# Kernel tuning notes

Measured on AMD Instinct MI355X. Metric: run time of the kernel, lower is better.

Reference implementation:

```python
import jax, jax.numpy as jnp
import numpy as np

N_NODES = 40000
N_EDGES = 320000
IN_DIM = 256
HID = 128
HEADS = 4
N_GAT = 3  # num_layers - 1
EPS = 1e-5
NEG_SLOPE = 0.2  # PyG GATConv default


def setup_inputs() -> dict:
    key = jax.random.key(0)
    ks = jax.random.split(key, 16)
    s = 0.05
    return {
        "x": jax.random.normal(ks[0], (N_NODES, IN_DIM), jnp.float32),
        "edge_index": jax.random.randint(ks[1], (2, N_EDGES), 0, N_NODES, jnp.int64),
        "proj_W": jax.random.normal(ks[2], (IN_DIM, HID), jnp.float32) * s,
        "proj_b": jnp.zeros((HID,), jnp.float32),
        "gat_W": jax.random.normal(ks[3], (N_GAT, HID, HEADS * HID), jnp.float32) * s,
        "gat_att_src": jax.random.normal(ks[4], (N_GAT, HEADS, HID), jnp.float32) * s,
        "gat_att_dst": jax.random.normal(ks[5], (N_GAT, HEADS, HID), jnp.float32) * s,
        "gat_bias": jnp.zeros((N_GAT, HID), jnp.float32),
        "ln_gamma": jnp.ones((N_GAT, HID), jnp.float32),
        "ln_beta": jnp.zeros((N_GAT, HID), jnp.float32),
        "gcn_W": jax.random.normal(ks[6], (HID, 1), jnp.float32) * s,
        "gcn_b": jnp.zeros((1,), jnp.float32),
    }


def reference(x, edge_index, proj_W, proj_b, gat_W, gat_att_src, gat_att_dst,
              gat_bias, ln_gamma, ln_beta, gcn_W, gcn_b):
    N = x.shape[0]
    loops = jnp.arange(N)
    src = jnp.concatenate([edge_index[0], loops])  # add_self_loops=True
    dst = jnp.concatenate([edge_index[1], loops])

    h = x @ proj_W + proj_b  # [N, HID]

    for i in range(N_GAT):
        identity = h
        xh = (h @ gat_W[i]).reshape(N, HEADS, HID)      # [N, H, C]
        a_s = jnp.einsum("nhc,hc->nh", xh, gat_att_src[i])  # [N, H]
        a_d = jnp.einsum("nhc,hc->nh", xh, gat_att_dst[i])
        e = jax.nn.leaky_relu(a_s[src] + a_d[dst], NEG_SLOPE)  # [E, H]
        # segment softmax over incoming edges per dst node
        m = jax.ops.segment_max(e, dst, num_segments=N)
        ex = jnp.exp(e - m[dst])
        denom = jax.ops.segment_sum(ex, dst, num_segments=N)
        alpha = ex / denom[dst]                         # [E, H]
        agg = jax.ops.segment_sum(xh[src] * alpha[:, :, None], dst, num_segments=N)
        h = agg.mean(axis=1) + gat_bias[i]              # concat=False -> head mean
        # LayerNorm (biased variance, eps=1e-5)
        mu = h.mean(-1, keepdims=True)
        var = ((h - mu) ** 2).mean(-1, keepdims=True)
        h = (h - mu) * jax.lax.rsqrt(var + EPS) * ln_gamma[i] + ln_beta[i]
        h = jax.nn.relu(h)
        # dropout: inference mode -> identity
        h = h + identity

    # GCNConv(hidden, 1) with symmetric normalization and self loops
    deg = jax.ops.segment_sum(jnp.ones_like(dst, dtype=h.dtype), dst, num_segments=N)
    dinv = jax.lax.rsqrt(deg)  # deg >= 1 due to self loops
    norm = dinv[src] * dinv[dst]                        # [E]
    xw = h @ gcn_W                                      # [N, 1]
    out = jax.ops.segment_sum(xw[src] * norm[:, None], dst, num_segments=N) + gcn_b
    return jax.nn.sigmoid(out).reshape(-1)
```

## Files before the change

kernel.cpp:

```cpp
#include <hip/hip_runtime.h>
#include <math.h>

#define INDIM 256
#define HID 128
#define HEADS 4
#define NGAT 3
#define LN_EPS 1e-5f
#define SLOPE 0.2f
#define MPAD 40064
#define LOG2E 1.4426950408889634f

typedef __attribute__((ext_vector_type(8))) short short8;
typedef __attribute__((ext_vector_type(4))) float f32x4;

__device__ inline float wsum(float v) {
#pragma unroll
  for (int m = 1; m < 64; m <<= 1) v += __shfl_xor(v, m, 64);
  return v;
}
__device__ inline float wmax(float v) {
#pragma unroll
  for (int m = 1; m < 64; m <<= 1) v = fmaxf(v, __shfl_xor(v, m, 64));
  return v;
}
__device__ inline float lk2(float v) { return fmaxf(v, SLOPE * v) * LOG2E; }
__device__ inline float sel4(float a0, float a1, float a2, float a3, int i) {
  float lo = (i & 1) ? a1 : a0;
  float hi = (i & 1) ? a3 : a2;
  return (i & 2) ? hi : lo;
}

__device__ inline unsigned short f2b(float f) {
  unsigned u = __float_as_uint(f);
  unsigned r = (u + 0x7FFFu + ((u >> 16) & 1u)) >> 16;
  return (unsigned short)r;
}
__device__ inline void unp8(const uint4 v, float f[8]) {
  f[0] = __uint_as_float(v.x << 16);
  f[1] = __uint_as_float(v.x & 0xFFFF0000u);
  f[2] = __uint_as_float(v.y << 16);
  f[3] = __uint_as_float(v.y & 0xFFFF0000u);
  f[4] = __uint_as_float(v.z << 16);
  f[5] = __uint_as_float(v.z & 0xFFFF0000u);
  f[6] = __uint_as_float(v.w << 16);
  f[7] = __uint_as_float(v.w & 0xFFFF0000u);
}

__device__ __host__ inline size_t fidx(int row, int k, int K) {
  return ((size_t)(row >> 4) * (K >> 5) + (k >> 5)) * 512 +
         ((((k >> 3) & 3) * 16 + (row & 15)) << 3) + (k & 7);
}

__global__ void k_deg(const int* __restrict__ ei, int E, int N, int* __restrict__ deg) {
  int e = blockIdx.x * blockDim.x + threadIdx.x;
  if (e >= E + N) return;
  int dst = (e < E) ? ei[E + e] : (e - E);
  atomicAdd(&deg[dst], 1);
}

__global__ void k_scan1(const int* __restrict__ deg, int N, int* __restrict__ bsums) {
  __shared__ int s[256];
  int gid = blockIdx.x * 256 + threadIdx.x;
  s[threadIdx.x] = (gid < N) ? deg[gid] : 0;
  __syncthreads();
  for (int off = 128; off > 0; off >>= 1) {
    if (threadIdx.x < off) s[threadIdx.x] += s[threadIdx.x + off];
    __syncthreads();
  }
  if (threadIdx.x == 0) bsums[blockIdx.x] = s[0];
}

__global__ void k_scan2(int* __restrict__ bsums, int nblk, int* __restrict__ rowptr, int N) {
  __shared__ int s[256];
  int t = threadIdx.x;
  int v = (t < nblk) ? bsums[t] : 0;
  s[t] = v;
  __syncthreads();
  for (int off = 1; off < 256; off <<= 1) {
    int u = (t >= off) ? s[t - off] : 0;
    __syncthreads();
    s[t] += u;
    __syncthreads();
  }
  if (t < nblk) bsums[t] = s[t] - v;
  if (t == nblk - 1) rowptr[N] = s[t];
}

__global__ void k_scan3(const int* __restrict__ deg, int N, const int* __restrict__ bsums,
                        int* __restrict__ rowptr, int* __restrict__ cursor,
                        float* __restrict__ dinv) {
  __shared__ int s[256];
  int gid = blockIdx.x * 256 + threadIdx.x;
  int v = (gid < N) ? deg[gid] : 0;
  s[threadIdx.x] = v;
  __syncthreads();
  for (int off = 1; off < 256; off <<= 1) {
    int t = (threadIdx.x >= off) ? s[threadIdx.x - off] : 0;
    __syncthreads();
    s[threadIdx.x] += t;
    __syncthreads();
  }
  if (gid < N) {
    int ex = bsums[blockIdx.x] + s[threadIdx.x] - v;
    rowptr[gid] = ex;
    cursor[gid] = ex;
    dinv[gid] = rsqrtf((float)v);
  }
}

__global__ void k_fill(const int* __restrict__ ei, int E, int N,
                       int* __restrict__ cursor, int* __restrict__ csr) {
  int e = blockIdx.x * blockDim.x + threadIdx.x;
  if (e >= E + N) return;
  int src, dst;
  if (e < E) { src = ei[e]; dst = ei[E + e]; } else { src = dst = e - E; }
  int pos = atomicAdd(&cursor[dst], 1);
  csr[pos] = src;
}

__global__ void k_wtp(const float* __restrict__ W, unsigned short* __restrict__ Wt) {
  int idx = blockIdx.x * 256 + threadIdx.x;
  if (idx >= INDIM * HID) return;
  int k = idx >> 7, c = idx & 127;
  Wt[fidx(c, k, INDIM)] = f2b(W[idx]);
}

__global__ void k_wt2(const float* __restrict__ W, unsigned short* __restrict__ Wt) {
  int idx = blockIdx.x * 256 + threadIdx.x;
  if (idx >= NGAT * HID * HEADS * HID) return;
  int l = idx / (HID * HEADS * HID);
  int rem = idx - l * HID * HEADS * HID;
  int k = rem >> 9;
  int cc = rem & 511;
  int hh = cc >> 7, c = cc & 127;
  Wt[(size_t)l * (HID * HEADS * HID) + fidx(c, hh * HID + k, HEADS * HID)] =
      f2b(W[idx] * 0.25f);
}

__global__ void k_xfrag(const float* __restrict__ x, unsigned short* __restrict__ xbF,
                        int N) {
  int t = blockIdx.x * 256 + threadIdx.x;
  if (t >= MPAD * 32) return;
  int n = t >> 5, kc = t & 31;
  uint4 pk = make_uint4(0, 0, 0, 0);
  if (n < N) {
    const float* ap = x + (size_t)n * INDIM + kc * 8;
    float4 u = *(const float4*)ap;
    float4 v = *(const float4*)(ap + 4);
    pk.x = (unsigned)f2b(u.x) | ((unsigned)f2b(u.y) << 16);
    pk.y = (unsigned)f2b(u.z) | ((unsigned)f2b(u.w) << 16);
    pk.z = (unsigned)f2b(v.x) | ((unsigned)f2b(v.y) << 16);
    pk.w = (unsigned)f2b(v.z) | ((unsigned)f2b(v.w) << 16);
  }
  size_t addr = ((size_t)(n >> 4) * 8 + (kc >> 2)) * 512 +
                (((kc & 3) * 16 + (n & 15)) << 3);
  *(uint4*)(xbF + addr) = pk;
}

__global__ void k_wvec(const float* __restrict__ W, const float* __restrict__ atts,
                       const float* __restrict__ attd, float* __restrict__ w_s,
                       float* __restrict__ w_d) {
  int lane = threadIdx.x & 63;
  int idx = blockIdx.x * 4 + (threadIdx.x >> 6);
  if (idx >= NGAT * HEADS * HID) return;
  int l = idx / (HEADS * HID);
  int rem = idx - l * (HEADS * HID);
  int hh = rem >> 7, k = rem & 127;
  const float2 w2 = *(const float2*)(W + ((size_t)(l * HID + k)) * (HEADS * HID) +
                                     hh * HID + lane * 2);
  const float2 s2 = *(const float2*)(atts + (size_t)(l * HEADS + hh) * HID + lane * 2);
  const float2 d2 = *(const float2*)(attd + (size_t)(l * HEADS + hh) * HID + lane * 2);
  float ps = w2.x * s2.x + w2.y * s2.y;
  float pd = w2.x * d2.x + w2.y * d2.y;
  ps = wsum(ps);
  pd = wsum(pd);
  if (lane == 0) { w_s[idx] = ps; w_d[idx] = pd; }
}

__global__ __launch_bounds__(256) void k_mm(
    const unsigned short* __restrict__ xbF, const unsigned short* __restrict__ WtPF,
    const float* __restrict__ bias, const float* __restrict__ ws0,
    const float* __restrict__ wd0, float* __restrict__ h,
    unsigned short* __restrict__ hb, float* __restrict__ a_s,
    float* __restrict__ a_d) {
  const int wid = threadIdx.x >> 6;
  const int lane = threadIdx.x & 63;
  const int l15 = lane & 15;
  const int g = lane >> 4;
  const int row0 = blockIdx.x * 64 + wid * 16;
  f32x4 acc[8] = {};
  const unsigned short* Ap = xbF + (size_t)(row0 >> 4) * 8 * 512 + lane * 8;
  const unsigned short* Bp = WtPF + lane * 8;
  for (int kb = 0; kb < 8; ++kb) {
    short8 af = *(const short8*)(Ap + kb * 512);
    short8 bfr[8];
#pragma unroll
    for (int ni = 0; ni < 8; ++ni)
      bfr[ni] = *(const short8*)(Bp + (size_t)(ni * 8 + kb) * 512);
#pragma unroll
    for (int ni = 0; ni < 8; ++ni)
      acc[ni] = __builtin_amdgcn_mfma_f32_16x16x32_bf16(af, bfr[ni], acc[ni], 0, 0, 0);
  }
#pragma unroll
  for (int r = 0; r < 4; ++r) {
    const int row = row0 + g * 4 + r;
    float* hr = h + (size_t)row * HID;
    unsigned short* hbr = hb + (size_t)row * HID;
    float yv[8];
#pragma unroll
    for (int ni = 0; ni < 8; ++ni) {
      const int c = ni * 16 + l15;
      yv[ni] = acc[ni][r] + bias[c];
      hr[c] = yv[ni];
      hbr[c] = f2b(yv[ni]);
    }
    float ps[4], pd[4];
#pragma unroll
    for (int h4 = 0; h4 < 4; ++h4) {
      float pv = 0.f, qv = 0.f;
#pragma unroll
      for (int ni = 0; ni < 8; ++ni) {
        const int c = h4 * HID + ni * 16 + l15;
        pv = fmaf(yv[ni], ws0[c], pv);
        qv = fmaf(yv[ni], wd0[c], qv);
      }
#pragma unroll
      for (int m = 1; m < 16; m <<= 1) {
        pv += __shfl_xor(pv, m, 64);
        qv += __shfl_xor(qv, m, 64);
      }
      ps[h4] = pv;
      pd[h4] = qv;
    }
    if (l15 == 0) {
      *(float4*)(a_s + (size_t)row * 4) = make_float4(ps[0], ps[1], ps[2], ps[3]);
      *(float4*)(a_d + (size_t)row * 4) = make_float4(pd[0], pd[1], pd[2], pd[3]);
    }
  }
}

__global__ __launch_bounds__(256) void k_agg2(
    const int* __restrict__ rowptr, const int* __restrict__ csr,
    const unsigned short* __restrict__ hb, const float* __restrict__ a_s,
    const float* __restrict__ a_d, unsigned short* __restrict__ aggF, int N) {
  __shared__ int s_lds[4][64];
  __shared__ float al_lds[4][4][68];
  int lane = threadIdx.x & 63;
  int wid = threadIdx.x >> 6;
  int n = blockIdx.x * 4 + wid;
  if (n >= N) return;
  int beg = rowptr[n], end = rowptr[n + 1];
  int deg = end - beg;
  const float4 adv = *(const float4*)(a_d + (size_t)n * 4);
  const int g = lane >> 4;
  const int l15 = lane & 15;
  const unsigned short* hbase = hb + l15 * 8;
  float acc[8] = {};
  float f[8];
  if (deg <= 64) {
    int e = beg + lane;
    bool val = e < end;
    int s = csr[val ? e : end - 1];
    const float4 asv = *(const float4*)(a_s + (size_t)s * 4);
    float L0 = lk2(asv.x + adv.x);
    float L1 = lk2(asv.y + adv.y);
    float L2 = lk2(asv.z + adv.z);
    float L3 = lk2(asv.w + adv.w);
    float m0 = wmax(val ? L0 : -3e38f);
    float m1 = wmax(val ? L1 : -3e38f);
    float m2 = wmax(val ? L2 : -3e38f);
    float m3 = wmax(val ? L3 : -3e38f);
    float e0 = val ? exp2f(L0 - m0) : 0.f;
    float e1 = val ? exp2f(L1 - m1) : 0.f;
    float e2 = val ? exp2f(L2 - m2) : 0.f;
    float e3 = val ? exp2f(L3 - m3) : 0.f;
    s_lds[wid][lane] = s;
    al_lds[wid][0][lane] = e0 / wsum(e0);
    al_lds[wid][1][lane] = e1 / wsum(e1);
    al_lds[wid][2][lane] = e2 / wsum(e2);
    al_lds[wid][3][lane] = e3 / wsum(e3);
    asm volatile("s_waitcnt lgkmcnt(0)" ::: "memory");
    const int* sw = s_lds[wid];
    const float* aw = al_lds[wid][g];
    int nIter = (deg + 3) >> 2;
    for (int it = 0; it < nIter; ++it) {
      int4 s4 = *(const int4*)(sw + it * 4);
      float4 a4 = *(const float4*)(aw + it * 4);
      uint4 r0 = *(const uint4*)(hbase + (size_t)s4.x * HID);
      uint4 r1 = *(const uint4*)(hbase + (size_t)s4.y * HID);
      uint4 r2 = *(const uint4*)(hbase + (size_t)s4.z * HID);
      uint4 r3 = *(const uint4*)(hbase + (size_t)s4.w * HID);
      unp8(r0, f);
#pragma unroll
      for (int j = 0; j < 8; ++j) acc[j] = fmaf(a4.x, f[j], acc[j]);
      unp8(r1, f);
#pragma unroll
      for (int j = 0; j < 8; ++j) acc[j] = fmaf(a4.y, f[j], acc[j]);
      unp8(r2, f);
#pragma unroll
      for (int j = 0; j < 8; ++j) acc[j] = fmaf(a4.z, f[j], acc[j]);
      unp8(r3, f);
#pragma unroll
      for (int j = 0; j < 8; ++j) acc[j] = fmaf(a4.w, f[j], acc[j]);
    }
  } else {
    float m0 = -3e38f, m1 = -3e38f, m2 = -3e38f, m3 = -3e38f;
    for (int e = beg + lane; e < end; e += 64) {
      int s = csr[e];
      const float4 asv = *(const float4*)(a_s + (size_t)s * 4);
      m0 = fmaxf(m0, lk2(asv.x + adv.x));
      m1 = fmaxf(m1, lk2(asv.y + adv.y));
      m2 = fmaxf(m2, lk2(asv.z + adv.z));
      m3 = fmaxf(m3, lk2(asv.w + adv.w));
    }
    m0 = wmax(m0); m1 = wmax(m1); m2 = wmax(m2); m3 = wmax(m3);
    float d0 = 0.f, d1 = 0.f, d2 = 0.f, d3 = 0.f;
    for (int e = beg + lane; e < end; e += 64) {
      int s = csr[e];
      const float4 asv = *(const float4*)(a_s + (size_t)s * 4);
      d0 += exp2f(lk2(asv.x + adv.x) - m0);
      d1 += exp2f(lk2(asv.y + adv.y) - m1);
      d2 += exp2f(lk2(asv.z + adv.z) - m2);
      d3 += exp2f(lk2(asv.w + adv.w) - m3);
    }
    float r0 = 1.f / wsum(d0);
    float r1 = 1.f / wsum(d1);
    float r2 = 1.f / wsum(d2);
    float r3 = 1.f / wsum(d3);
    for (int sb = beg; sb < end; sb += 64) {
      int e = sb + lane;
      bool val = e < end;
      int s = csr[val ? e : end - 1];
      const float4 asv = *(const float4*)(a_s + (size_t)s * 4);
      float q0 = val ? exp2f(lk2(asv.x + adv.x) - m0) * r0 : 0.f;
      float q1 = val ? exp2f(lk2(asv.y + adv.y) - m1) * r1 : 0.f;
      float q2 = val ? exp2f(lk2(asv.z + adv.z) - m2) * r2 : 0.f;
      float q3 = val ? exp2f(lk2(asv.w + adv.w) - m3) * r3 : 0.f;
      int cnt = min(64, end - sb);
      for (int i = 0; i < cnt; ++i) {
        int si = __shfl(s, i, 64);
        float c0 = __shfl(q0, i, 64), c1 = __shfl(q1, i, 64);
        float c2 = __shfl(q2, i, 64), c3 = __shfl(q3, i, 64);
        uint4 hv = *(const uint4*)(hbase + (size_t)si * HID);
        float bi = sel4(c0, c1, c2, c3, g);
        unp8(hv, f);
#pragma unroll
        for (int j = 0; j < 8; ++j) acc[j] = fmaf(bi, f[j], acc[j]);
      }
    }
  }
  uint4 pk;
  pk.x = (unsigned)f2b(acc[0]) | ((unsigned)f2b(acc[1]) << 16);
  pk.y = (unsigned)f2b(acc[2]) | ((unsigned)f2b(acc[3]) << 16);
  pk.z = (unsigned)f2b(acc[4]) | ((unsigned)f2b(acc[5]) << 16);
  pk.w = (unsigned)f2b(acc[6]) | ((unsigned)f2b(acc[7]) << 16);
  size_t addr = ((size_t)(n >> 4) * 16 + (g * 4 + (l15 >> 2))) * 512 +
                (((l15 & 3) * 16 + (n & 15)) << 3);
  *(uint4*)(aggF + addr) = pk;
}

template <int ATT>
__global__ __launch_bounds__(256) void k_mm2(
    const unsigned short* __restrict__ aggF, const unsigned short* __restrict__ Bt,
    const float* __restrict__ bias, const float* __restrict__ gamma,
    const float* __restrict__ beta, const float* __restrict__ wsn,
    const float* __restrict__ wdn, float* __restrict__ h,
    unsigned short* __restrict__ hb, float* __restrict__ a_s,
    float* __restrict__ a_d, float* __restrict__ xw) {
  const int wid = threadIdx.x >> 6;
  const int lane = threadIdx.x & 63;
  const int l15 = lane & 15;
  const int g = lane >> 4;
  const int row0 = blockIdx.x * 64 + wid * 16;
  f32x4 acc[8] = {};
  const unsigned short* Ap = aggF + (size_t)(row0 >> 4) * 16 * 512 + lane * 8;
  const unsigned short* Bp = Bt + lane * 8;
  for (int kb = 0; kb < 16; ++kb) {
    short8 a0 = *(const short8*)(Ap + kb * 512);
    short8 bfr[8];
#pragma unroll
    for (int ni = 0; ni < 8; ++ni)
      bfr[ni] = *(const short8*)(Bp + (size_t)(ni * 16 + kb) * 512);
#pragma unroll
    for (int ni = 0; ni < 8; ++ni)
      acc[ni] = __builtin_amdgcn_mfma_f32_16x16x32_bf16(a0, bfr[ni], acc[ni], 0, 0, 0);
  }
  float gm[8], bt8[8];
#pragma unroll
  for (int ni = 0; ni < 8; ++ni) {
    int c = ni * 16 + l15;
    gm[ni] = gamma[c];
    bt8[ni] = beta[c];
    float bs = bias[c];
#pragma unroll
    for (int r = 0; r < 4; ++r) acc[ni][r] += bs;
  }
#pragma unroll
  for (int r = 0; r < 4; ++r) {
    float s = 0.f;
#pragma unroll
    for (int ni = 0; ni < 8; ++ni) s += acc[ni][r];
#pragma unroll
    for (int m = 1; m < 16; m <<= 1) s += __shfl_xor(s, m, 64);
    float mu = s * (1.f / 128.f);
    float q = 0.f;
#pragma unroll
    for (int ni = 0; ni < 8; ++ni) {
      float dd = acc[ni][r] - mu;
      q += dd * dd;
    }
#pragma unroll
    for (int m = 1; m < 16; m <<= 1) q += __shfl_xor(q, m, 64);
    float rstd = rsqrtf(q * (1.f / 128.f) + LN_EPS);
    const int row = row0 + g * 4 + r;
    float* hr = h + (size_t)row * HID;
    unsigned short* hbr = hb + (size_t)row * HID;
    float yv[8];
#pragma unroll
    for (int ni = 0; ni < 8; ++ni) {
      int c = ni * 16 + l15;
      float y = (acc[ni][r] - mu) * rstd * gm[ni] + bt8[ni];
      y = fmaxf(y, 0.f) + hr[c];
      hr[c] = y;
      hbr[c] = f2b(y);
      yv[ni] = y;
    }
    if (ATT == 1) {
      float ps[4], pd[4];
#pragma unroll
      for (int h4 = 0; h4 < 4; ++h4) {
        float pv = 0.f, qv = 0.f;
#pragma unroll
        for (int ni = 0; ni < 8; ++ni) {
          const int c = h4 * HID + ni * 16 + l15;
          pv = fmaf(yv[ni], wsn[c], pv);
          qv = fmaf(yv[ni], wdn[c], qv);
        }
#pragma unroll
        for (int m = 1; m < 16; m <<= 1) {
          pv += __shfl_xor(pv, m, 64);
          qv += __shfl_xor(qv, m, 64);
        }
        ps[h4] = pv;
        pd[h4] = qv;
      }
      if (l15 == 0) {
        *(float4*)(a_s + (size_t)row * 4) = make_float4(ps[0], ps[1], ps[2], ps[3]);
        *(float4*)(a_d + (size_t)row * 4) = make_float4(pd[0], pd[1], pd[2], pd[3]);
      }
    } else {
      float pv = 0.f;
#pragma unroll
      for (int ni = 0; ni < 8; ++ni) pv = fmaf(yv[ni], wsn[ni * 16 + l15], pv);
#pragma unroll
      for (int m = 1; m < 16; m <<= 1) pv += __shfl_xor(pv, m, 64);
      if (l15 == 0) xw[row] = pv;
    }
  }
}

__global__ __launch_bounds__(256) void k_gcn(const int* __restrict__ rowptr,
                                             const int* __restrict__ csr,
                                             const float* __restrict__ xw,
                                             const float* __restrict__ dinv,
                                             const float* __restrict__ gcn_b,
                                             float* __restrict__ out, int N) {
  int n = blockIdx.x * blockDim.x + threadIdx.x;
  if (n >= N) return;
  float acc = 0.f;
  int beg = rowptr[n], end = rowptr[n + 1];
  for (int e = beg; e < end; ++e) {
    int s = csr[e];
    acc += xw[s] * dinv[s];
  }
  float z = acc * dinv[n] + gcn_b[0];
  out[n] = 1.f / (1.f + expf(-z));
}

extern "C" void kernel_launch(void* const* d_in, const int* in_sizes, int n_in,
                              void* d_out, int out_size, void* d_ws, size_t ws_size,
                              hipStream_t stream) {
  const float* x = (const float*)d_in[0];
  const int* ei = (const int*)d_in[1];
  const float* proj_W = (const float*)d_in[2];
  const float* proj_b = (const float*)d_in[3];
  const float* gat_W = (const float*)d_in[4];
  const float* gat_as = (const float*)d_in[5];
  const float* gat_ad = (const float*)d_in[6];
  const float* gat_bias = (const float*)d_in[7];
  const float* ln_g = (const float*)d_in[8];
  const float* ln_b = (const float*)d_in[9];
  const float* gcn_W = (const float*)d_in[10];
  const float* gcn_b = (const float*)d_in[11];
  float* out = (float*)d_out;

  const int N = in_sizes[0] / INDIM;
  const int E = in_sizes[1] / 2;
  const int TOT = E + N;

  size_t off = 0;
  auto alloc = [&](size_t bytes) {
    void* p = (char*)d_ws + off;
    off += (bytes + 255) & ~(size_t)255;
    return p;
  };
  float* h = (float*)alloc((size_t)MPAD * HID * 4);
  unsigned short* hb = (unsigned short*)alloc((size_t)MPAD * HID * 2);
  unsigned short* aggF = (unsigned short*)alloc((size_t)MPAD * HEADS * HID * 2);
  unsigned short* xbF = (unsigned short*)alloc((size_t)MPAD * INDIM * 2);
  unsigned short* WtPF = (unsigned short*)alloc((size_t)HID * INDIM * 2);
  unsigned short* Wt2F = (unsigned short*)alloc((size_t)NGAT * HID * HEADS * HID * 2);
  float* w_s = (float*)alloc((size_t)NGAT * HEADS * HID * 4);
  float* w_d = (float*)alloc((size_t)NGAT * HEADS * HID * 4);
  float* a_s = (float*)alloc((size_t)MPAD * HEADS * 4);
  float* a_d = (float*)alloc((size_t)MPAD * HEADS * 4);
  int* deg = (int*)alloc((size_t)N * 4);
  int* rowptr = (int*)alloc((size_t)(N + 1) * 4);
  int* cursor = (int*)alloc((size_t)N * 4);
  int* csr = (int*)alloc((size_t)TOT * 4);
  int* bsums = (int*)alloc(1024);
  float* dinv = (float*)alloc((size_t)N * 4);
  float* xw = (float*)alloc((size_t)MPAD * 4);
  (void)ws_size;

  const int NBLK = (N + 255) / 256;
  const int EBLK = (TOT + 255) / 256;
  const int WBLK = (N + 3) / 4;

  hipMemsetAsync(deg, 0, (size_t)N * 4, stream);
  k_deg<<<EBLK, 256, 0, stream>>>(ei, E, N, deg);
  k_scan1<<<NBLK, 256, 0, stream>>>(deg, N, bsums);
  k_scan2<<<1, 256, 0, stream>>>(bsums, NBLK, rowptr, N);
  k_scan3<<<NBLK, 256, 0, stream>>>(deg, N, bsums, rowptr, cursor, dinv);
  k_fill<<<EBLK, 256, 0, stream>>>(ei, E, N, cursor, csr);

  k_wtp<<<(INDIM * HID + 255) / 256, 256, 0, stream>>>(proj_W, WtPF);
  k_wt2<<<(NGAT * HID * HEADS * HID + 255) / 256, 256, 0, stream>>>(gat_W, Wt2F);
  k_wvec<<<(NGAT * HEADS * HID + 3) / 4, 256, 0, stream>>>(gat_W, gat_as, gat_ad, w_s, w_d);
  k_xfrag<<<(MPAD * 32 + 255) / 256, 256, 0, stream>>>(x, xbF, N);

  hipMemsetAsync(aggF + (size_t)N * HEADS * HID, 0,
                 (size_t)(MPAD - N) * HEADS * HID * 2, stream);

  k_mm<<<MPAD / 64, 256, 0, stream>>>(xbF, WtPF, proj_b, w_s, w_d, h, hb, a_s, a_d);

  for (int i = 0; i < NGAT; ++i) {
    k_agg2<<<WBLK, 256, 0, stream>>>(rowptr, csr, hb, a_s, a_d, aggF, N);
    if (i < NGAT - 1) {
      k_mm2<1><<<MPAD / 64, 256, 0, stream>>>(
          aggF, Wt2F + (size_t)i * HID * HEADS * HID, gat_bias + (size_t)i * HID,
          ln_g + (size_t)i * HID, ln_b + (size_t)i * HID,
          w_s + (size_t)(i + 1) * HEADS * HID, w_d + (size_t)(i + 1) * HEADS * HID,
          h, hb, a_s, a_d, nullptr);
    } else {
      k_mm2<2><<<MPAD / 64, 256, 0, stream>>>(
          aggF, Wt2F + (size_t)i * HID * HEADS * HID, gat_bias + (size_t)i * HID,
          ln_g + (size_t)i * HID, ln_b + (size_t)i * HID, gcn_W, nullptr,
          h, hb, nullptr, nullptr, xw);
    }
  }

  k_gcn<<<NBLK, 256, 0, stream>>>(rowptr, csr, xw, dinv, gcn_b, out, N);
}
```

Baseline: 293.9 us.

## Split GAT aggregation into separate attention-softmax and feature-gather kernels

Replaces the fused per-node softmax+aggregation kernel with two kernels: one computes per-edge, per-head attention weights with one thread per (node, head) and writes them to a new global buffer, and a second gathers the bf16 source features weighted by those stored alphas. It also folds the two weight-preparation kernels into one launch and replaces the padding memset with zero writes from the gather kernel. This removes the wave-wide shuffles and LDS staging from the gather path but adds an extra launch per layer, a round trip of alphas through global memory, and serial per-thread loops over the edge list that reread csr and a_s three times.

```diff
diff --git a/kernel.cpp b/kernel.cpp
--- a/kernel.cpp
+++ b/kernel.cpp
@@ -18,17 +18,7 @@
   for (int m = 1; m < 64; m <<= 1) v += __shfl_xor(v, m, 64);
   return v;
 }
-__device__ inline float wmax(float v) {
-#pragma unroll
-  for (int m = 1; m < 64; m <<= 1) v = fmaxf(v, __shfl_xor(v, m, 64));
-  return v;
-}
 __device__ inline float lk2(float v) { return fmaxf(v, SLOPE * v) * LOG2E; }
-__device__ inline float sel4(float a0, float a1, float a2, float a3, int i) {
-  float lo = (i & 1) ? a1 : a0;
-  float hi = (i & 1) ? a3 : a2;
-  return (i & 2) ? hi : lo;
-}
 
 __device__ inline unsigned short f2b(float f) {
   unsigned u = __float_as_uint(f);
@@ -118,23 +108,24 @@
   csr[pos] = src;
 }
 
-__global__ void k_wtp(const float* __restrict__ W, unsigned short* __restrict__ Wt) {
+__global__ void k_wprep(const float* __restrict__ Wp, const float* __restrict__ Wg,
+                        unsigned short* __restrict__ WtPF,
+                        unsigned short* __restrict__ Wt2F) {
   int idx = blockIdx.x * 256 + threadIdx.x;
-  if (idx >= INDIM * HID) return;
-  int k = idx >> 7, c = idx & 127;
-  Wt[fidx(c, k, INDIM)] = f2b(W[idx]);
-}
-
-__global__ void k_wt2(const float* __restrict__ W, unsigned short* __restrict__ Wt) {
-  int idx = blockIdx.x * 256 + threadIdx.x;
+  if (idx < INDIM * HID) {
+    int k = idx >> 7, c = idx & 127;
+    WtPF[fidx(c, k, INDIM)] = f2b(Wp[idx]);
+    return;
+  }
+  idx -= INDIM * HID;
   if (idx >= NGAT * HID * HEADS * HID) return;
   int l = idx / (HID * HEADS * HID);
   int rem = idx - l * HID * HEADS * HID;
   int k = rem >> 9;
   int cc = rem & 511;
   int hh = cc >> 7, c = cc & 127;
-  Wt[(size_t)l * (HID * HEADS * HID) + fidx(c, hh * HID + k, HEADS * HID)] =
-      f2b(W[idx] * 0.25f);
+  Wt2F[(size_t)l * (HID * HEADS * HID) + fidx(c, hh * HID + k, HEADS * HID)] =
+      f2b(Wg[idx] * 0.25f);
 }
 
 __global__ void k_xfrag(const float* __restrict__ x, unsigned short* __restrict__ xbF,
@@ -239,123 +230,83 @@
   }
 }
 
-__global__ __launch_bounds__(256) void k_agg2(
+__global__ __launch_bounds__(256) void k_alpha(
     const int* __restrict__ rowptr, const int* __restrict__ csr,
-    const unsigned short* __restrict__ hb, const float* __restrict__ a_s,
-    const float* __restrict__ a_d, unsigned short* __restrict__ aggF, int N) {
-  __shared__ int s_lds[4][64];
-  __shared__ float al_lds[4][4][68];
+    const float* __restrict__ a_s, const float* __restrict__ a_d,
+    float* __restrict__ alf, int N) {
+  int t = blockIdx.x * 256 + threadIdx.x;
+  int n = t >> 2, h = t & 3;
+  if (n >= N) return;
+  int beg = rowptr[n], end = rowptr[n + 1];
+  float ad = a_d[n * 4 + h];
+  float m = -3e38f;
+  for (int e = beg; e < end; ++e)
+    m = fmaxf(m, lk2(a_s[csr[e] * 4 + h] + ad));
+  float d = 0.f;
+  for (int e = beg; e < end; ++e)
+    d += exp2f(lk2(a_s[csr[e] * 4 + h] + ad) - m);
+  float r = 1.f / d;
+  for (int e = beg; e < end; ++e)
+    alf[e * 4 + h] = exp2f(lk2(a_s[csr[e] * 4 + h] + ad) - m) * r;
+}
+
+__global__ __launch_bounds__(256) void k_gather(
+    const int* __restrict__ rowptr, const int* __restrict__ csr,
+    const unsigned short* __restrict__ hb, const float* __restrict__ alf,
+    unsigned short* __restrict__ aggF, int N) {
   int lane = threadIdx.x & 63;
   int wid = threadIdx.x >> 6;
   int n = blockIdx.x * 4 + wid;
-  if (n >= N) return;
-  int beg = rowptr[n], end = rowptr[n + 1];
-  int deg = end - beg;
-  const float4 adv = *(const float4*)(a_d + (size_t)n * 4);
+  if (n >= MPAD) return;
   const int g = lane >> 4;
   const int l15 = lane & 15;
+  size_t addr = ((size_t)(n >> 4) * 16 + (g * 4 + (l15 >> 2))) * 512 +
+                (((l15 & 3) * 16 + (n & 15)) << 3);
+  if (n >= N) {
+    *(uint4*)(aggF + addr) = make_uint4(0, 0, 0, 0);
+    return;
+  }
+  int beg = rowptr[n], end = rowptr[n + 1];
   const unsigned short* hbase = hb + l15 * 8;
   float acc[8] = {};
   float f[8];
-  if (deg <= 64) {
-    int e = beg + lane;
-    bool val = e < end;
-    int s = csr[val ? e : end - 1];
-    const float4 asv = *(const float4*)(a_s + (size_t)s * 4);
-    float L0 = lk2(asv.x + adv.x);
-    float L1 = lk2(asv.y + adv.y);
-    float L2 = lk2(asv.z + adv.z);
-    float L3 = lk2(asv.w + adv.w);
-    float m0 = wmax(val ? L0 : -3e38f);
-    float m1 = wmax(val ? L1 : -3e38f);
-    float m2 = wmax(val ? L2 : -3e38f);
-    float m3 = wmax(val ? L3 : -3e38f);
-    float e0 = val ? exp2f(L0 - m0) : 0.f;
-    float e1 = val ? exp2f(L1 - m1) : 0.f;
-    float e2 = val ? exp2f(L2 - m2) : 0.f;
-    float e3 = val ? exp2f(L3 - m3) : 0.f;
-    s_lds[wid][lane] = s;
-    al_lds[wid][0][lane] = e0 / wsum(e0);
-    al_lds[wid][1][lane] = e1 / wsum(e1);
-    al_lds[wid][2][lane] = e2 / wsum(e2);
-    al_lds[wid][3][lane] = e3 / wsum(e3);
-    asm volatile("s_waitcnt lgkmcnt(0)" ::: "memory");
-    const int* sw = s_lds[wid];
-    const float* aw = al_lds[wid][g];
-    int nIter = (deg + 3) >> 2;
-    for (int it = 0; it < nIter; ++it) {
-      int4 s4 = *(const int4*)(sw + it * 4);
-      float4 a4 = *(const float4*)(aw + it * 4);
-      uint4 r0 = *(const uint4*)(hbase + (size_t)s4.x * HID);
-      uint4 r1 = *(const uint4*)(hbase + (size_t)s4.y * HID);
-      uint4 r2 = *(const uint4*)(hbase + (size_t)s4.z * HID);
-      uint4 r3 = *(const uint4*)(hbase + (size_t)s4.w * HID);
-      unp8(r0, f);
-#pragma unroll
-      for (int j = 0; j < 8; ++j) acc[j] = fmaf(a4.x, f[j], acc[j]);
-      unp8(r1, f);
-#pragma unroll
-      for (int j = 0; j < 8; ++j) acc[j] = fmaf(a4.y, f[j], acc[j]);
-      unp8(r2, f);
-#pragma unroll
-      for (int j = 0; j < 8; ++j) acc[j] = fmaf(a4.z, f[j], acc[j]);
-      unp8(r3, f);
-#pragma unroll
-      for (int j = 0; j < 8; ++j) acc[j] = fmaf(a4.w, f[j], acc[j]);
-    }
-  } else {
-    float m0 = -3e38f, m1 = -3e38f, m2 = -3e38f, m3 = -3e38f;
-    for (int e = beg + lane; e < end; e += 64) {
-      int s = csr[e];
-      const float4 asv = *(const float4*)(a_s + (size_t)s * 4);
-      m0 = fmaxf(m0, lk2(asv.x + adv.x));
-      m1 = fmaxf(m1, lk2(asv.y + adv.y));
-      m2 = fmaxf(m2, lk2(asv.z + adv.z));
-      m3 = fmaxf(m3, lk2(asv.w + adv.w));
-    }
-    m0 = wmax(m0); m1 = wmax(m1); m2 = wmax(m2); m3 = wmax(m3);
-    float d0 = 0.f, d1 = 0.f, d2 = 0.f, d3 = 0.f;
-    for (int e = beg + lane; e < end; e += 64) {
-      int s = csr[e];
-      const float4 asv = *(const float4*)(a_s + (size_t)s * 4);
-      d0 += exp2f(lk2(asv.x + adv.x) - m0);
-      d1 += exp2f(lk2(asv.y + adv.y) - m1);
-      d2 += exp2f(lk2(asv.z + adv.z) - m2);
-      d3 += exp2f(lk2(asv.w + adv.w) - m3);
-    }
-    float r0 = 1.f / wsum(d0);
-    float r1 = 1.f / wsum(d1);
-    float r2 = 1.f / wsum(d2);
-    float r3 = 1.f / wsum(d3);
-    for (int sb = beg; sb < end; sb += 64) {
-      int e = sb + lane;
-      bool val = e < end;
-      int s = csr[val ? e : end - 1];
-      const float4 asv = *(const float4*)(a_s + (size_t)s * 4);
-      float q0 = val ? exp2f(lk2(asv.x + adv.x) - m0) * r0 : 0.f;
-      float q1 = val ? exp2f(lk2(asv.y + adv.y) - m1) * r1 : 0.f;
-      float q2 = val ? exp2f(lk2(asv.z + adv.z) - m2) * r2 : 0.f;
-      float q3 = val ? exp2f(lk2(asv.w + adv.w) - m3) * r3 : 0.f;
-      int cnt = min(64, end - sb);
-      for (int i = 0; i < cnt; ++i) {
-        int si = __shfl(s, i, 64);
-        float c0 = __shfl(q0, i, 64), c1 = __shfl(q1, i, 64);
-        float c2 = __shfl(q2, i, 64), c3 = __shfl(q3, i, 64);
-        uint4 hv = *(const uint4*)(hbase + (size_t)si * HID);
-        float bi = sel4(c0, c1, c2, c3, g);
-        unp8(hv, f);
-#pragma unroll
-        for (int j = 0; j < 8; ++j) acc[j] = fmaf(bi, f[j], acc[j]);
-      }
-    }
+  int e = beg;
+  for (; e + 4 <= end; e += 4) {
+    int s0 = csr[e], s1 = csr[e + 1], s2 = csr[e + 2], s3 = csr[e + 3];
+    float a0 = alf[e * 4 + g];
+    float a1 = alf[(e + 1) * 4 + g];
+    float a2 = alf[(e + 2) * 4 + g];
+    float a3 = alf[(e + 3) * 4 + g];
+    uint4 r0 = *(const uint4*)(hbase + (size_t)s0 * HID);
+    uint4 r1 = *(const uint4*)(hbase + (size_t)s1 * HID);
+    uint4 r2 = *(const uint4*)(hbase + (size_t)s2 * HID);
+    uint4 r3 = *(const uint4*)(hbase + (size_t)s3 * HID);
+    unp8(r0, f);
+#pragma unroll
+    for (int j = 0; j < 8; ++j) acc[j] = fmaf(a0, f[j], acc[j]);
+    unp8(r1, f);
+#pragma unroll
+    for (int j = 0; j < 8; ++j) acc[j] = fmaf(a1, f[j], acc[j]);
+    unp8(r2, f);
+#pragma unroll
+    for (int j = 0; j < 8; ++j) acc[j] = fmaf(a2, f[j], acc[j]);
+    unp8(r3, f);
+#pragma unroll
+    for (int j = 0; j < 8; ++j) acc[j] = fmaf(a3, f[j], acc[j]);
+  }
+  for (; e < end; ++e) {
+    int s0 = csr[e];
+    float a0 = alf[e * 4 + g];
+    uint4 r0 = *(const uint4*)(hbase + (size_t)s0 * HID);
+    unp8(r0, f);
+#pragma unroll
+    for (int j = 0; j < 8; ++j) acc[j] = fmaf(a0, f[j], acc[j]);
   }
   uint4 pk;
   pk.x = (unsigned)f2b(acc[0]) | ((unsigned)f2b(acc[1]) << 16);
   pk.y = (unsigned)f2b(acc[2]) | ((unsigned)f2b(acc[3]) << 16);
   pk.z = (unsigned)f2b(acc[4]) | ((unsigned)f2b(acc[5]) << 16);
   pk.w = (unsigned)f2b(acc[6]) | ((unsigned)f2b(acc[7]) << 16);
-  size_t addr = ((size_t)(n >> 4) * 16 + (g * 4 + (l15 >> 2))) * 512 +
-                (((l15 & 3) * 16 + (n & 15)) << 3);
   *(uint4*)(aggF + addr) = pk;
 }
 
@@ -514,6 +465,7 @@
   float* w_d = (float*)alloc((size_t)NGAT * HEADS * HID * 4);
   float* a_s = (float*)alloc((size_t)MPAD * HEADS * 4);
   float* a_d = (float*)alloc((size_t)MPAD * HEADS * 4);
+  float* alf = (float*)alloc((size_t)TOT * HEADS * 4);
   int* deg = (int*)alloc((size_t)N * 4);
   int* rowptr = (int*)alloc((size_t)(N + 1) * 4);
   int* cursor = (int*)alloc((size_t)N * 4);
@@ -525,7 +477,6 @@
 
   const int NBLK = (N + 255) / 256;
   const int EBLK = (TOT + 255) / 256;
-  const int WBLK = (N + 3) / 4;
 
   hipMemsetAsync(deg, 0, (size_t)N * 4, stream);
   k_deg<<<EBLK, 256, 0, stream>>>(ei, E, N, deg);
@@ -534,18 +485,16 @@
   k_scan3<<<NBLK, 256, 0, stream>>>(deg, N, bsums, rowptr, cursor, dinv);
   k_fill<<<EBLK, 256, 0, stream>>>(ei, E, N, cursor, csr);
 
-  k_wtp<<<(INDIM * HID + 255) / 256, 256, 0, stream>>>(proj_W, WtPF);
-  k_wt2<<<(NGAT * HID * HEADS * HID + 255) / 256, 256, 0, stream>>>(gat_W, Wt2F);
+  const int WPN = INDIM * HID + NGAT * HID * HEADS * HID;
+  k_wprep<<<(WPN + 255) / 256, 256, 0, stream>>>(proj_W, gat_W, WtPF, Wt2F);
   k_wvec<<<(NGAT * HEADS * HID + 3) / 4, 256, 0, stream>>>(gat_W, gat_as, gat_ad, w_s, w_d);
   k_xfrag<<<(MPAD * 32 + 255) / 256, 256, 0, stream>>>(x, xbF, N);
 
-  hipMemsetAsync(aggF + (size_t)N * HEADS * HID, 0,
-                 (size_t)(MPAD - N) * HEADS * HID * 2, stream);
-
   k_mm<<<MPAD / 64, 256, 0, stream>>>(xbF, WtPF, proj_b, w_s, w_d, h, hb, a_s, a_d);
 
   for (int i = 0; i < NGAT; ++i) {
-    k_agg2<<<WBLK, 256, 0, stream>>>(rowptr, csr, hb, a_s, a_d, aggF, N);
+    k_alpha<<<(N * 4 + 255) / 256, 256, 0, stream>>>(rowptr, csr, a_s, a_d, alf, N);
+    k_gather<<<MPAD / 4, 256, 0, stream>>>(rowptr, csr, hb, alf, aggF, N);
     if (i < NGAT - 1) {
       k_mm2<1><<<MPAD / 64, 256, 0, stream>>>(
           aggF, Wt2F + (size_t)i * HID * HEADS * HID, gat_bias + (size_t)i * HID,
```

After: 343.4 us. 16.8% more time.
